# Kernel optimization log

Measured on AMD Instinct MI355X. Metric: run time of the kernel, lower is better.

The kernel has to match this reference:

```python
import jax, jax.numpy as jnp
import numpy as np

B, T, C, H = 4, 4096, 1024, 64  # batch, seq, input_size, head_size


def setup_inputs() -> dict:
    key = jax.random.key(0)
    ks = jax.random.split(key, 7)
    s = 1.0 / np.sqrt(C)  # nn.Linear default init scale (uniform +-1/sqrt(fan_in))
    return {
        "x": jax.random.normal(ks[0], (B, T, C), dtype=jnp.float32),
        "Wk": jax.random.uniform(ks[1], (C, H), jnp.float32, -s, s),
        "bk": jax.random.uniform(ks[2], (H,), jnp.float32, -s, s),
        "Wq": jax.random.uniform(ks[3], (C, H), jnp.float32, -s, s),
        "bq": jax.random.uniform(ks[4], (H,), jnp.float32, -s, s),
        "Wv": jax.random.uniform(ks[5], (C, H), jnp.float32, -s, s),
        "bv": jax.random.uniform(ks[6], (H,), jnp.float32, -s, s),
    }


def reference(x, Wk, bk, Wq, bq, Wv, bv):
    b, t, c = x.shape
    k = x @ Wk + bk            # [B,T,H]
    q = x @ Wq + bq            # [B,T,H]
    v = x @ Wv + bv            # [B,T,H]
    # NOTE: original scales by C**-0.5 (input dim), not head_size**-0.5
    wei = jnp.einsum("bqh,bkh->bqk", q, k) * (c ** -0.5)  # [B,T,T]
    causal = jnp.tril(jnp.ones((t, t), dtype=bool))
    wei = jnp.where(causal, wei, -jnp.inf)
    wei = jax.nn.softmax(wei, axis=-1)
    # dropout p=0.0 (eval-mode baseline) -> identity
    return wei @ v             # [B,T,H]
```

## Files before the change

kernel.cpp:

```cpp
#include <hip/hip_runtime.h>

#define B_ 4
#define T_ 4096
#define C_ 1024
#define H_ 64
#define QSCALE 0.045084220027780106f

typedef float  f32x4  __attribute__((ext_vector_type(4)));
typedef __bf16 bf16x8 __attribute__((ext_vector_type(8)));
typedef __bf16 bf16x4 __attribute__((ext_vector_type(4)));

#define MFMA16(a, b, c) __builtin_amdgcn_mfma_f32_16x16x32_bf16((a), (b), (c), 0, 0, 0)

__device__ __forceinline__ void gl16(const void* g, void* l) {
    __builtin_amdgcn_global_load_lds(
        (const __attribute__((address_space(1))) void*)g,
        (__attribute__((address_space(3))) void*)l, 16, 0, 0);
}

#define CPB 187
#define NCHUNK 6

__global__ __launch_bounds__(256) void prep_wt(const float* __restrict__ Wk,
                                               const float* __restrict__ Wq,
                                               const float* __restrict__ Wv,
                                               __bf16* __restrict__ Wt) {
    __shared__ float tile[16][65];
    int tid = threadIdx.x;
    int mat = blockIdx.x >> 6;
    int k0  = (blockIdx.x & 63) * 16;
    const float* W = (mat == 0) ? Wk : ((mat == 1) ? Wq : Wv);
#pragma unroll
    for (int i = 0; i < 4; ++i) {
        int e = i * 256 + tid;
        int ki = e >> 6, n = e & 63;
        tile[ki][n] = W[(size_t)(k0 + ki) * 64 + n];
    }
    __syncthreads();
#pragma unroll
    for (int i = 0; i < 4; ++i) {
        int e = i * 256 + tid;
        int n = e >> 4, kj = e & 15;
        Wt[(size_t)mat * 65536 + (size_t)n * 1024 + k0 + kj] = (__bf16)tile[kj][n];
    }
}

#define STAGE(xd, wd, kk) do {                                              \
    const char* xs_ = xsrc + (size_t)(kk) * 4;                              \
    gl16(xs_,          (xd) + wq * 1024);                                   \
    gl16(xs_ + 65536,  (xd) + 4096 + wq * 1024);                            \
    const char* ws_ = wsrc + (size_t)(kk) * 2;                              \
    gl16(ws_,           (wd) + wq * 1024);                                  \
    gl16(ws_ + 65536,   (wd) + 4096  + wq * 1024);                          \
    gl16(ws_ + 131072,  (wd) + 8192  + wq * 1024);                          \
    gl16(ws_ + 196608,  (wd) + 12288 + wq * 1024);                          \
    gl16(ws_ + 262144,  (wd) + 16384 + wq * 1024);                          \
    gl16(ws_ + 327680,  (wd) + 20480 + wq * 1024);                          \
} while (0)

__global__ __launch_bounds__(256) void proj_qkv(const float* __restrict__ x,
                                                const __bf16* __restrict__ Wt,
                                                const float* __restrict__ bk,
                                                const float* __restrict__ bq,
                                                const float* __restrict__ bv,
                                                __bf16* __restrict__ Kg,
                                                __bf16* __restrict__ Qg,
                                                __bf16* __restrict__ Vt) {
    __shared__ char smem[65536];

    int tid  = threadIdx.x;
    int wq   = tid >> 6;
    int lane = tid & 63;
    int lo = lane & 15, g = lane >> 4;
    int swz = lo & 7;
    int w2 = wq >> 1, wc = wq & 1;
    int r0 = w2 * 16, n0 = wc * 96;
    int row0 = blockIdx.x * 32;

    const char* xsrc = (const char*)(x + (size_t)(row0 + (tid >> 4)) * C_
                                       + (size_t)(((tid & 15) ^ ((tid >> 4) & 7)) * 4));
    const char* wsrc = (const char*)Wt + (size_t)(tid >> 3) * 2048
                                       + (size_t)(((tid & 7) ^ ((tid >> 3) & 7)) * 16);

    char* xcur = smem;          char* xnxt = smem + 8192;
    char* wcur = smem + 16384;  char* wnxt = smem + 40960;

    f32x4 acc[6];
#pragma unroll
    for (int nt = 0; nt < 6; ++nt) acc[nt] = (f32x4){0.f, 0.f, 0.f, 0.f};

    STAGE(xcur, wcur, 0);
    __syncthreads();

#pragma unroll 1
    for (int step = 0; step < 16; ++step) {
        if (step < 15) STAGE(xnxt, wnxt, (step + 1) * 64);

        bf16x8 af[2];
        const char* ap = xcur + (r0 + lo) * 256;
#pragma unroll
        for (int kc = 0; kc < 2; ++kc) {
            int ch0 = kc * 8 + g * 2;
            f32x4 a0 = *(const f32x4*)(ap + ((ch0)     ^ swz) * 16);
            f32x4 a1 = *(const f32x4*)(ap + ((ch0 + 1) ^ swz) * 16);
            bf16x8 t;
            t[0] = (__bf16)a0[0]; t[1] = (__bf16)a0[1];
            t[2] = (__bf16)a0[2]; t[3] = (__bf16)a0[3];
            t[4] = (__bf16)a1[0]; t[5] = (__bf16)a1[1];
            t[6] = (__bf16)a1[2]; t[7] = (__bf16)a1[3];
            af[kc] = t;
        }
#pragma unroll
        for (int nt = 0; nt < 6; ++nt) {
            const char* bp_ = wcur + (n0 + nt * 16 + lo) * 128;
#pragma unroll
            for (int kc = 0; kc < 2; ++kc) {
                bf16x8 bf_ = *(const bf16x8*)(bp_ + ((kc * 4 + g) ^ swz) * 16);
                acc[nt] = MFMA16(af[kc], bf_, acc[nt]);
            }
        }
        __syncthreads();
        char* t1 = xcur; xcur = xnxt; xnxt = t1;
        char* t2 = wcur; wcur = wnxt; wnxt = t2;
    }

    int b_   = row0 >> 12;
    int tloc = row0 & (T_ - 1);
#pragma unroll
    for (int nt = 0; nt < 6; ++nt) {
        int col = n0 + nt * 16 + lo;
        int mat = col >> 6, h = col & 63;
        const float* bp = (mat == 0) ? bk : ((mat == 1) ? bq : bv);
        float bb = bp[h];
        if (mat == 2) {
            bf16x4 pv;
#pragma unroll
            for (int r = 0; r < 4; ++r) pv[r] = (__bf16)(acc[nt][r] + bb);
            *(bf16x4*)(Vt + (size_t)(b_ * 64 + h) * T_ + tloc + r0 + 4 * g) = pv;
        } else if (mat == 1) {
#pragma unroll
            for (int r = 0; r < 4; ++r)
                Qg[(size_t)(row0 + r0 + 4 * g + r) * H_ + h] = (__bf16)((acc[nt][r] + bb) * QSCALE);
        } else {
#pragma unroll
            for (int r = 0; r < 4; ++r)
                Kg[(size_t)(row0 + r0 + 4 * g + r) * H_ + h] = (__bf16)(acc[nt][r] + bb);
        }
    }
}

__device__ __forceinline__ void attn_iter_lds(const char* __restrict__ kb_,
                                              const char* __restrict__ vb_,
                                              int k0abs, int q0, bool domask,
                                              bf16x8 qb0, bf16x8 qb1,
                                              f32x4 (&acc)[4], float& m, float& l,
                                              char* pl, int lo, int g) {
    f32x4 st[4];
#pragma unroll
    for (int kt = 0; kt < 4; ++kt) {
        int row = kt * 16 + lo, sw = row & 7;
        bf16x8 ka0 = *(const bf16x8*)(kb_ + row * 128 + ((g ^ sw) << 4));
        bf16x8 ka1 = *(const bf16x8*)(kb_ + row * 128 + (((g + 4) ^ sw) << 4));
        f32x4 z = (f32x4){0.f, 0.f, 0.f, 0.f};
        __builtin_amdgcn_s_setprio(1);
        z = MFMA16(ka0, qb0, z);
        z = MFMA16(ka1, qb1, z);
        __builtin_amdgcn_s_setprio(0);
        st[kt] = z;
    }
    if (domask) {
#pragma unroll
        for (int kt = 0; kt < 4; ++kt)
#pragma unroll
            for (int r = 0; r < 4; ++r) {
                int kabs = k0abs + kt * 16 + 4 * g + r;
                if (kabs > q0 + lo) st[kt][r] = -1e30f;
            }
    }
    float mloc = -1e30f;
#pragma unroll
    for (int kt = 0; kt < 4; ++kt)
#pragma unroll
        for (int r = 0; r < 4; ++r) mloc = fmaxf(mloc, st[kt][r]);
    mloc = fmaxf(mloc, __shfl_xor(mloc, 16));
    mloc = fmaxf(mloc, __shfl_xor(mloc, 32));
    float mnew  = fmaxf(m, mloc);
    float alpha = exp2f(m - mnew);
    float ls = 0.f;
#pragma unroll
    for (int kt = 0; kt < 4; ++kt)
#pragma unroll
        for (int r = 0; r < 4; ++r) {
            float pe = exp2f(st[kt][r] - mnew);
            st[kt][r] = pe;
            ls += pe;
        }
    ls += __shfl_xor(ls, 16);
    ls += __shfl_xor(ls, 32);
    l = l * alpha + ls;
    m = mnew;
#pragma unroll
    for (int r = 0; r < 4; ++r) {
        float ar = __shfl(alpha, 4 * g + r);
#pragma unroll
        for (int ht = 0; ht < 4; ++ht) acc[ht][r] *= ar;
    }
#pragma unroll
    for (int kt = 0; kt < 4; ++kt) {
        bf16x4 pk;
#pragma unroll
        for (int r = 0; r < 4; ++r) pk[r] = (__bf16)st[kt][r];
        int waddr = (lo * 128 + kt * 32 + g * 8) ^ ((lo & 7) << 4);
        *(bf16x4*)(pl + waddr) = pk;
    }
#pragma unroll
    for (int c2 = 0; c2 < 2; ++c2) {
        int raddr = (lo * 128 + c2 * 64 + g * 16) ^ ((lo & 7) << 4);
        bf16x8 pa = *(const bf16x8*)(pl + raddr);
        __builtin_amdgcn_s_setprio(1);
#pragma unroll
        for (int ht = 0; ht < 4; ++ht) {
            int row = ht * 16 + lo, sw = row & 7;
            bf16x8 vb = *(const bf16x8*)(vb_ + row * 128 + (((c2 * 4 + g) ^ sw) << 4));
            acc[ht] = MFMA16(pa, vb, acc[ht]);
        }
        __builtin_amdgcn_s_setprio(0);
    }
}

__global__ __launch_bounds__(512) void attn_fwd(const __bf16* __restrict__ Qg,
                                                const __bf16* __restrict__ Kg,
                                                const __bf16* __restrict__ Vt,
                                                __bf16* __restrict__ partO,
                                                float* __restrict__ partML) {
    __shared__ alignas(16) char smem[49152];

    int tid  = threadIdx.x;
    int w    = tid >> 6;
    int lane = tid & 63;
    int lo = lane & 15, gq = lane >> 4;

    int bid = blockIdx.x;
    int b   = bid / CPB;
    int u   = bid - b * CPB;
    int g = 0, cum = 0;
#pragma unroll 1
    for (; g < 32; ++g) {
        int s = (2 * g + 7) / 6;
        if (u < cum + s) break;
        cum += s;
    }
    int c    = u - cum;
    int j0   = NCHUNK * c;
    int cnt  = min(NCHUNK, 2 * g + 2 - j0);
    int mydiag = 2 * g + (w >> 2);
    int q0   = g * 128 + w * 16;

    const char* kgb = (const char*)Kg + (size_t)b * 524288;
    const char* vgb = (const char*)Vt + (size_t)b * 524288;

    int sr = tid >> 3;
    int sc2 = (tid & 7) ^ (sr & 7);
    int koff = sr * 128 + sc2 * 16;
    int voff = sr * 8192 + sc2 * 16;
    char* pl = smem + 32768 + w * 2048;

    const __bf16* qp = Qg + (size_t)(b * T_ + q0 + lo) * H_ + gq * 8;
    bf16x8 qb0 = *(const bf16x8*)(qp);
    bf16x8 qb1 = *(const bf16x8*)(qp + 32);

    f32x4 acc[4];
#pragma unroll
    for (int ht = 0; ht < 4; ++ht) acc[ht] = (f32x4){0.f, 0.f, 0.f, 0.f};
    float m = -1e30f, l = 0.f;

    gl16(kgb + (size_t)j0 * 8192 + koff, smem + w * 1024);
    gl16(vgb + (size_t)j0 * 128 + voff, smem + 16384 + w * 1024);
    __syncthreads();

#pragma unroll 1
    for (int t = 0; t < cnt; ++t) {
        int cur = t & 1;
        if (t + 1 < cnt) {
            int kb = j0 + t + 1;
            gl16(kgb + (size_t)kb * 8192 + koff, smem + (cur ^ 1) * 8192 + w * 1024);
            gl16(vgb + (size_t)kb * 128 + voff, smem + 16384 + (cur ^ 1) * 8192 + w * 1024);
        }
        int kb = j0 + t;
        if (kb <= mydiag) {
            attn_iter_lds(smem + cur * 8192, smem + 16384 + cur * 8192,
                          kb * 64, q0, kb == mydiag,
                          qb0, qb1, acc, m, l, pl, lo, gq);
        }
        __syncthreads();
    }

    __bf16* po = partO + (size_t)bid * 8192;
#pragma unroll
    for (int ht = 0; ht < 4; ++ht)
#pragma unroll
        for (int r = 0; r < 4; ++r)
            po[(w * 16 + 4 * gq + r) * 64 + ht * 16 + lo] = (__bf16)acc[ht][r];
    if (gq == 0) {
        partML[bid * 256 + (w * 16 + lo) * 2 + 0] = m;
        partML[bid * 256 + (w * 16 + lo) * 2 + 1] = l;
    }
}

__global__ __launch_bounds__(256) void mergeN(const __bf16* __restrict__ partO,
                                              const float* __restrict__ partML,
                                              float* __restrict__ out) {
    int e = blockIdx.x * 256 + threadIdx.x;
    int row = e >> 6, h = e & 63;
    int b = row >> 12, rl = row & 4095;
    int g = rl >> 7, r128 = rl & 127;
    int cum = 0;
#pragma unroll 1
    for (int gg = 0; gg < g; ++gg) cum += (2 * gg + 7) / 6;
    int S = (2 * g + 7) / 6;
    int base = b * CPB + cum;

    float M = -1e30f;
#pragma unroll 1
    for (int c2 = 0; c2 < S; ++c2)
        M = fmaxf(M, partML[(base + c2) * 256 + r128 * 2]);
    float L = 0.f, O = 0.f;
#pragma unroll 1
    for (int c2 = 0; c2 < S; ++c2) {
        float mc = partML[(base + c2) * 256 + r128 * 2];
        float lc = partML[(base + c2) * 256 + r128 * 2 + 1];
        float sc = exp2f(mc - M);
        L += lc * sc;
        O += (float)partO[(size_t)(base + c2) * 8192 + r128 * 64 + h] * sc;
    }
    out[e] = O / L;
}

extern "C" void kernel_launch(void* const* d_in, const int* in_sizes, int n_in,
                              void* d_out, int out_size, void* d_ws, size_t ws_size,
                              hipStream_t stream) {
    const float* x  = (const float*)d_in[0];
    const float* Wk = (const float*)d_in[1];
    const float* bk = (const float*)d_in[2];
    const float* Wq = (const float*)d_in[3];
    const float* bq = (const float*)d_in[4];
    const float* Wv = (const float*)d_in[5];
    const float* bv = (const float*)d_in[6];

    char* ws = (char*)d_ws;
    __bf16* Wt = (__bf16*)(ws);
    __bf16* Kg = (__bf16*)(ws + 393216);
    __bf16* Qg = (__bf16*)(ws + 393216 + 2097152);
    __bf16* Vt = (__bf16*)(ws + 393216 + 2 * 2097152);
    __bf16* partO  = (__bf16*)(ws + 6684672);
    float*  partML = (float*)(ws + 6684672 + 12255232);
    float* out = (float*)d_out;

    prep_wt<<<192, 256, 0, stream>>>(Wk, Wq, Wv, Wt);
    proj_qkv<<<512, 256, 0, stream>>>(x, Wt, bk, bq, bv, Kg, Qg, Vt);
    attn_fwd<<<4 * CPB, 512, 0, stream>>>(Qg, Kg, Vt, partO, partML);
    mergeN<<<4096, 256, 0, stream>>>(partO, partML, out);
}
```

Before: 66.63 us.

## Read V from global in attention, double projection tile, one-pass merge

The attention kernel stops staging V tiles in LDS and has each wave load V fragments straight from global memory. This shrinks shared memory and raises the launch-bound occupancy hint, at the cost of all eight waves redundantly fetching the same V tile through the cache. The projection kernel now runs 512 threads on 64-row tiles with the staging pattern adjusted to match. The merge kernel replaces its two passes over the partials with a single online-rescaling pass that also loads each m/l pair with one vector load.

```diff
diff --git a/kernel.cpp b/kernel.cpp
--- a/kernel.cpp
+++ b/kernel.cpp
@@ -7,6 +7,7 @@
 #define QSCALE 0.045084220027780106f
 
 typedef float  f32x4  __attribute__((ext_vector_type(4)));
+typedef float  f32x2  __attribute__((ext_vector_type(2)));
 typedef __bf16 bf16x8 __attribute__((ext_vector_type(8)));
 typedef __bf16 bf16x4 __attribute__((ext_vector_type(4)));
 
@@ -47,18 +48,15 @@
 
 #define STAGE(xd, wd, kk) do {                                              \
     const char* xs_ = xsrc + (size_t)(kk) * 4;                              \
-    gl16(xs_,          (xd) + wq * 1024);                                   \
-    gl16(xs_ + 65536,  (xd) + 4096 + wq * 1024);                            \
+    gl16(xs_,           (xd) + wq * 1024);                                  \
+    gl16(xs_ + 131072,  (xd) + 8192 + wq * 1024);                           \
     const char* ws_ = wsrc + (size_t)(kk) * 2;                              \
     gl16(ws_,           (wd) + wq * 1024);                                  \
-    gl16(ws_ + 65536,   (wd) + 4096  + wq * 1024);                          \
     gl16(ws_ + 131072,  (wd) + 8192  + wq * 1024);                          \
-    gl16(ws_ + 196608,  (wd) + 12288 + wq * 1024);                          \
     gl16(ws_ + 262144,  (wd) + 16384 + wq * 1024);                          \
-    gl16(ws_ + 327680,  (wd) + 20480 + wq * 1024);                          \
 } while (0)
 
-__global__ __launch_bounds__(256) void proj_qkv(const float* __restrict__ x,
+__global__ __launch_bounds__(512) void proj_qkv(const float* __restrict__ x,
                                                 const __bf16* __restrict__ Wt,
                                                 const float* __restrict__ bk,
                                                 const float* __restrict__ bq,
@@ -66,7 +64,7 @@
                                                 __bf16* __restrict__ Kg,
                                                 __bf16* __restrict__ Qg,
                                                 __bf16* __restrict__ Vt) {
-    __shared__ char smem[65536];
+    __shared__ char smem[81920];
 
     int tid  = threadIdx.x;
     int wq   = tid >> 6;
@@ -75,15 +73,15 @@
     int swz = lo & 7;
     int w2 = wq >> 1, wc = wq & 1;
     int r0 = w2 * 16, n0 = wc * 96;
-    int row0 = blockIdx.x * 32;
+    int row0 = blockIdx.x * 64;
 
     const char* xsrc = (const char*)(x + (size_t)(row0 + (tid >> 4)) * C_
                                        + (size_t)(((tid & 15) ^ ((tid >> 4) & 7)) * 4));
     const char* wsrc = (const char*)Wt + (size_t)(tid >> 3) * 2048
                                        + (size_t)(((tid & 7) ^ ((tid >> 3) & 7)) * 16);
 
-    char* xcur = smem;          char* xnxt = smem + 8192;
-    char* wcur = smem + 16384;  char* wnxt = smem + 40960;
+    char* xcur = smem;          char* xnxt = smem + 16384;
+    char* wcur = smem + 32768;  char* wnxt = smem + 57344;
 
     f32x4 acc[6];
 #pragma unroll
@@ -150,7 +148,7 @@
 }
 
 __device__ __forceinline__ void attn_iter_lds(const char* __restrict__ kb_,
-                                              const char* __restrict__ vb_,
+                                              const __bf16* __restrict__ vtB,
                                               int k0abs, int q0, bool domask,
                                               bf16x8 qb0, bf16x8 qb1,
                                               f32x4 (&acc)[4], float& m, float& l,
@@ -220,20 +218,20 @@
         __builtin_amdgcn_s_setprio(1);
 #pragma unroll
         for (int ht = 0; ht < 4; ++ht) {
-            int row = ht * 16 + lo, sw = row & 7;
-            bf16x8 vb = *(const bf16x8*)(vb_ + row * 128 + (((c2 * 4 + g) ^ sw) << 4));
+            bf16x8 vb = *(const bf16x8*)(vtB + (size_t)(ht * 16 + lo) * T_
+                                         + k0abs + c2 * 32 + g * 8);
             acc[ht] = MFMA16(pa, vb, acc[ht]);
         }
         __builtin_amdgcn_s_setprio(0);
     }
 }
 
-__global__ __launch_bounds__(512) void attn_fwd(const __bf16* __restrict__ Qg,
-                                                const __bf16* __restrict__ Kg,
-                                                const __bf16* __restrict__ Vt,
-                                                __bf16* __restrict__ partO,
-                                                float* __restrict__ partML) {
-    __shared__ alignas(16) char smem[49152];
+__global__ __launch_bounds__(512, 8) void attn_fwd(const __bf16* __restrict__ Qg,
+                                                   const __bf16* __restrict__ Kg,
+                                                   const __bf16* __restrict__ Vt,
+                                                   __bf16* __restrict__ partO,
+                                                   float* __restrict__ partML) {
+    __shared__ alignas(16) char smem[32768];
 
     int tid  = threadIdx.x;
     int w    = tid >> 6;
@@ -257,13 +255,12 @@
     int q0   = g * 128 + w * 16;
 
     const char* kgb = (const char*)Kg + (size_t)b * 524288;
-    const char* vgb = (const char*)Vt + (size_t)b * 524288;
+    const __bf16* vtB = Vt + (size_t)b * 32768 * 8;
 
     int sr = tid >> 3;
     int sc2 = (tid & 7) ^ (sr & 7);
     int koff = sr * 128 + sc2 * 16;
-    int voff = sr * 8192 + sc2 * 16;
-    char* pl = smem + 32768 + w * 2048;
+    char* pl = smem + 16384 + w * 2048;
 
     const __bf16* qp = Qg + (size_t)(b * T_ + q0 + lo) * H_ + gq * 8;
     bf16x8 qb0 = *(const bf16x8*)(qp);
@@ -275,21 +272,17 @@
     float m = -1e30f, l = 0.f;
 
     gl16(kgb + (size_t)j0 * 8192 + koff, smem + w * 1024);
-    gl16(vgb + (size_t)j0 * 128 + voff, smem + 16384 + w * 1024);
     __syncthreads();
 
 #pragma unroll 1
     for (int t = 0; t < cnt; ++t) {
         int cur = t & 1;
-        if (t + 1 < cnt) {
-            int kb = j0 + t + 1;
-            gl16(kgb + (size_t)kb * 8192 + koff, smem + (cur ^ 1) * 8192 + w * 1024);
-            gl16(vgb + (size_t)kb * 128 + voff, smem + 16384 + (cur ^ 1) * 8192 + w * 1024);
-        }
+        if (t + 1 < cnt)
+            gl16(kgb + (size_t)(j0 + t + 1) * 8192 + koff,
+                 smem + (cur ^ 1) * 8192 + w * 1024);
         int kb = j0 + t;
         if (kb <= mydiag) {
-            attn_iter_lds(smem + cur * 8192, smem + 16384 + cur * 8192,
-                          kb * 64, q0, kb == mydiag,
+            attn_iter_lds(smem + cur * 8192, vtB, kb * 64, q0, kb == mydiag,
                           qb0, qb1, acc, m, l, pl, lo, gq);
         }
         __syncthreads();
@@ -320,18 +313,16 @@
     int S = (2 * g + 7) / 6;
     int base = b * CPB + cum;
 
-    float M = -1e30f;
-#pragma unroll 1
-    for (int c2 = 0; c2 < S; ++c2)
-        M = fmaxf(M, partML[(base + c2) * 256 + r128 * 2]);
-    float L = 0.f, O = 0.f;
+    float M = -1e30f, L = 0.f, O = 0.f;
 #pragma unroll 1
     for (int c2 = 0; c2 < S; ++c2) {
-        float mc = partML[(base + c2) * 256 + r128 * 2];
-        float lc = partML[(base + c2) * 256 + r128 * 2 + 1];
-        float sc = exp2f(mc - M);
-        L += lc * sc;
-        O += (float)partO[(size_t)(base + c2) * 8192 + r128 * 64 + h] * sc;
+        f32x2 mlv = *(const f32x2*)(partML + (base + c2) * 256 + r128 * 2);
+        float oc = (float)partO[(size_t)(base + c2) * 8192 + r128 * 64 + h];
+        float Mn = fmaxf(M, mlv[0]);
+        float s0 = exp2f(M - Mn), s1 = exp2f(mlv[0] - Mn);
+        L = L * s0 + mlv[1] * s1;
+        O = O * s0 + oc * s1;
+        M = Mn;
     }
     out[e] = O / L;
 }
@@ -357,7 +348,7 @@
     float* out = (float*)d_out;
 
     prep_wt<<<192, 256, 0, stream>>>(Wk, Wq, Wv, Wt);
-    proj_qkv<<<512, 256, 0, stream>>>(x, Wt, bk, bq, bv, Kg, Qg, Vt);
+    proj_qkv<<<256, 512, 0, stream>>>(x, Wt, bk, bq, bv, Kg, Qg, Vt);
     attn_fwd<<<4 * CPB, 512, 0, stream>>>(Qg, Kg, Vt, partO, partML);
     mergeN<<<4096, 256, 0, stream>>>(partO, partML, out);
 }
```

Result: slower. 101.9 us (+53.0%).

## Triple-buffer K/V tiles with vmcnt waits and single-pass online merge

Applied to the files above, without the earlier changes.

The attention kernel moves from double to triple buffering of K/V tiles in LDS. It prefetches two tiles ahead and uses explicit s_waitcnt vmcnt plus one barrier per iteration instead of a trailing __syncthreads, so loads overlap compute more deeply. LDS use grows from 48KB to 64KB per block, which may reduce occupancy. The merge kernel now uses a single-pass online-softmax rescale with a vectorized m/l load instead of two passes over partML, at the cost of an extra exp per chunk.

```diff
diff --git a/kernel.cpp b/kernel.cpp
--- a/kernel.cpp
+++ b/kernel.cpp
@@ -7,6 +7,7 @@
 #define QSCALE 0.045084220027780106f
 
 typedef float  f32x4  __attribute__((ext_vector_type(4)));
+typedef float  f32x2  __attribute__((ext_vector_type(2)));
 typedef __bf16 bf16x8 __attribute__((ext_vector_type(8)));
 typedef __bf16 bf16x4 __attribute__((ext_vector_type(4)));
 
@@ -233,7 +234,7 @@
                                                 const __bf16* __restrict__ Vt,
                                                 __bf16* __restrict__ partO,
                                                 float* __restrict__ partML) {
-    __shared__ alignas(16) char smem[49152];
+    __shared__ alignas(16) char smem[65536];
 
     int tid  = threadIdx.x;
     int w    = tid >> 6;
@@ -263,7 +264,7 @@
     int sc2 = (tid & 7) ^ (sr & 7);
     int koff = sr * 128 + sc2 * 16;
     int voff = sr * 8192 + sc2 * 16;
-    char* pl = smem + 32768 + w * 2048;
+    char* pl = smem + 49152 + w * 2048;
 
     const __bf16* qp = Qg + (size_t)(b * T_ + q0 + lo) * H_ + gq * 8;
     bf16x8 qb0 = *(const bf16x8*)(qp);
@@ -275,24 +276,29 @@
     float m = -1e30f, l = 0.f;
 
     gl16(kgb + (size_t)j0 * 8192 + koff, smem + w * 1024);
-    gl16(vgb + (size_t)j0 * 128 + voff, smem + 16384 + w * 1024);
-    __syncthreads();
+    gl16(vgb + (size_t)j0 * 128 + voff, smem + 8192 + w * 1024);
+    if (cnt > 1) {
+        gl16(kgb + (size_t)(j0 + 1) * 8192 + koff, smem + 16384 + w * 1024);
+        gl16(vgb + (size_t)(j0 + 1) * 128 + voff, smem + 16384 + 8192 + w * 1024);
+    }
 
 #pragma unroll 1
     for (int t = 0; t < cnt; ++t) {
-        int cur = t & 1;
-        if (t + 1 < cnt) {
-            int kb = j0 + t + 1;
-            gl16(kgb + (size_t)kb * 8192 + koff, smem + (cur ^ 1) * 8192 + w * 1024);
-            gl16(vgb + (size_t)kb * 128 + voff, smem + 16384 + (cur ^ 1) * 8192 + w * 1024);
+        if (t + 1 < cnt) asm volatile("s_waitcnt vmcnt(2)" ::: "memory");
+        else             asm volatile("s_waitcnt vmcnt(0)" ::: "memory");
+        __builtin_amdgcn_s_barrier();
+        __builtin_amdgcn_sched_barrier(0);
+        if (t + 2 < cnt) {
+            int kb2 = j0 + t + 2;
+            char* nb = smem + ((t + 2) % 3) * 16384;
+            gl16(kgb + (size_t)kb2 * 8192 + koff, nb + w * 1024);
+            gl16(vgb + (size_t)kb2 * 128 + voff, nb + 8192 + w * 1024);
         }
         int kb = j0 + t;
-        if (kb <= mydiag) {
-            attn_iter_lds(smem + cur * 8192, smem + 16384 + cur * 8192,
-                          kb * 64, q0, kb == mydiag,
+        const char* kb_ = smem + (t % 3) * 16384;
+        if (kb <= mydiag)
+            attn_iter_lds(kb_, kb_ + 8192, kb * 64, q0, kb == mydiag,
                           qb0, qb1, acc, m, l, pl, lo, gq);
-        }
-        __syncthreads();
     }
 
     __bf16* po = partO + (size_t)bid * 8192;
@@ -320,18 +326,16 @@
     int S = (2 * g + 7) / 6;
     int base = b * CPB + cum;
 
-    float M = -1e30f;
-#pragma unroll 1
-    for (int c2 = 0; c2 < S; ++c2)
-        M = fmaxf(M, partML[(base + c2) * 256 + r128 * 2]);
-    float L = 0.f, O = 0.f;
+    float M = -1e30f, L = 0.f, O = 0.f;
 #pragma unroll 1
     for (int c2 = 0; c2 < S; ++c2) {
-        float mc = partML[(base + c2) * 256 + r128 * 2];
-        float lc = partML[(base + c2) * 256 + r128 * 2 + 1];
-        float sc = exp2f(mc - M);
-        L += lc * sc;
-        O += (float)partO[(size_t)(base + c2) * 8192 + r128 * 64 + h] * sc;
+        f32x2 mlv = *(const f32x2*)(partML + (base + c2) * 256 + r128 * 2);
+        float oc = (float)partO[(size_t)(base + c2) * 8192 + r128 * 64 + h];
+        float Mn = fmaxf(M, mlv[0]);
+        float s0 = exp2f(M - Mn), s1 = exp2f(mlv[0] - Mn);
+        L = L * s0 + mlv[1] * s1;
+        O = O * s0 + oc * s1;
+        M = Mn;
     }
     out[e] = O / L;
 }
```

Measured after the change: 67.15 us. No clear change (+0.8%).
